# Optimization experiments

Hardware: AMD Instinct MI355X
Metric: run time of the kernel (lower is better)

The kernel has to match this reference:

```python
import jax, jax.numpy as jnp
import numpy as np

EMBED_DIM = 1024
NUM_HEADS = 16
HEAD_DIM = EMBED_DIM // NUM_HEADS

def setup_inputs() -> dict:
    key = jax.random.key(0)
    k1, k2, k3 = jax.random.split(key, 3)
    x = jax.random.normal(k1, (4, 2048, EMBED_DIM), dtype=jnp.float32)
    # Linear weights stored as [out, in] like torch; we apply x @ W.T
    W_qkv = jax.random.normal(k2, (3 * EMBED_DIM, EMBED_DIM), dtype=jnp.float32) * (EMBED_DIM ** -0.5)
    W_proj = jax.random.normal(k3, (EMBED_DIM, EMBED_DIM), dtype=jnp.float32) * (EMBED_DIM ** -0.5)
    return {"x": x, "W_qkv": W_qkv, "W_proj": W_proj}

def reference(x, W_qkv, W_proj):
    B, T, C = x.shape
    H, D = NUM_HEADS, HEAD_DIM
    qkv = x @ W_qkv.T                          # [B,T,3C]
    q, k, v = jnp.split(qkv, 3, axis=-1)
    q = q.reshape(B, T, H, D).transpose(0, 2, 1, 3)  # [B,H,T,D]
    k = k.reshape(B, T, H, D).transpose(0, 2, 1, 3)
    v = v.reshape(B, T, H, D).transpose(0, 2, 1, 3)
    scores = jnp.einsum('bhqd,bhkd->bhqk', q, k) / jnp.sqrt(jnp.asarray(D, x.dtype))
    causal = jnp.tril(jnp.ones((T, T), dtype=bool))
    scores = jnp.where(causal, scores, -jnp.inf)
    weights = jax.nn.softmax(scores, axis=-1)
    out = jnp.einsum('bhqk,bhkd->bhqd', weights, v)  # [B,H,T,D]
    out = out.transpose(0, 2, 1, 3).reshape(B, T, C)
    return out @ W_proj.T
```

## Files before the change

### kernel.cpp

```cpp
#include <hip/hip_runtime.h>

#define T_SEQ 2048
#define NB 4
#define NH 16
#define HD 64
#define CDIM 1024
#define MROWS (NB * T_SEQ)

typedef __attribute__((ext_vector_type(8))) short short8;
typedef __attribute__((ext_vector_type(4))) float floatx4;

static __device__ __forceinline__ unsigned short f2bf(float f) {
  union { float f; unsigned int i; } c; c.f = f;
  return (unsigned short)((c.i + 0x7FFFu + ((c.i >> 16) & 1u)) >> 16);
}
static __device__ __forceinline__ unsigned short f2bf_trunc(float f) {
  union { float f; unsigned int i; } c; c.f = f;
  return (unsigned short)(c.i >> 16);
}

static __device__ __forceinline__ void gl2lds16(const void* g, void* l) {
  __builtin_amdgcn_global_load_lds(
      (const __attribute__((address_space(1))) unsigned int*)g,
      (__attribute__((address_space(3))) unsigned int*)l, 16, 0, 0);
}

#define X4 (MROWS * CDIM / 4)
#define WQ4 (3 * CDIM * CDIM / 4)
#define WP4 (CDIM * CDIM / 4)
__global__ __launch_bounds__(256) void cast3_bf16(const float* __restrict__ x,
                                                  const float* __restrict__ wq,
                                                  const float* __restrict__ wp,
                                                  unsigned short* __restrict__ out) {
  const int i = blockIdx.x * 256 + threadIdx.x;
  const float* src; int off;
  if (i < X4) { src = x; off = i; }
  else if (i < X4 + WQ4) { src = wq; off = i - X4; }
  else { src = wp; off = i - X4 - WQ4; }
  const float4 v = ((const float4*)src)[off];
  ushort4 o;
  o.x = f2bf(v.x); o.y = f2bf(v.y); o.z = f2bf(v.z); o.w = f2bf(v.w);
  ((ushort4*)out)[i] = o;
}

#define Q_PRESCALE 0.18033688f

#define QNT (CDIM / 64)

__global__ __launch_bounds__(512, 2) void gemm_bf16_qkv256(
    const unsigned short* __restrict__ A,
    const unsigned short* __restrict__ B,
    unsigned short* __restrict__ Oq,
    unsigned short* __restrict__ Ok,
    unsigned short* __restrict__ Ovt,
    const int K)
{
  __shared__ __align__(16) unsigned short As[2][2][128 * 64];
  __shared__ __align__(16) unsigned short Bs[2][2][128 * 64];
  const int tid = threadIdx.x;
  const int w = tid >> 6, l = tid & 63;
  const int quad = l >> 4, l15 = l & 15;
  const int wr = w >> 2, wc = w & 3;
  const int lin = blockIdx.y * 12 + blockIdx.x;
  const int swz = (lin & 7) * 48 + (lin >> 3);
  const int m0 = (swz / 12) * 256, n0 = (swz % 12) * 256;

  const int lrow = l >> 3;
  const int lch = ((l & 7) ^ lrow) * 8;
  const unsigned short* Ag = A + (size_t)(m0 + w * 16 + lrow) * K + lch;
  const unsigned short* Bg = B + (size_t)(n0 + w * 16 + lrow) * K + lch;
  const int ld0 = w * 1024, ld1 = w * 1024 + 512;
  const size_t rsk = (size_t)8 * K;

#define STAGE_A(buf, h, kof) do { \
    gl2lds16(Ag + (size_t)(h) * 128 * K + (kof), &As[buf][h][ld0]); \
    gl2lds16(Ag + (size_t)(h) * 128 * K + rsk + (kof), &As[buf][h][ld1]); } while (0)
#define STAGE_B(buf, h, kof) do { \
    gl2lds16(Bg + (size_t)(h) * 128 * K + (kof), &Bs[buf][h][ld0]); \
    gl2lds16(Bg + (size_t)(h) * 128 * K + rsk + (kof), &Bs[buf][h][ld1]); } while (0)

  const int sw7 = l15 & 7;
  const int co0 = (quad ^ sw7) * 8;
  const int co1 = co0 ^ 32;
  const int fb = l15 * 64;
  const unsigned short* Aw0 = &As[0][wr][0];
  const unsigned short* Aw1 = &As[1][wr][0];
  const unsigned short* Bw0 = &Bs[0][wc >> 1][(wc & 1) * 4096];
  const unsigned short* Bw1 = &Bs[1][wc >> 1][(wc & 1) * 4096];

  floatx4 acc[8][4];
#pragma unroll
  for (int mi = 0; mi < 8; ++mi)
#pragma unroll
    for (int ni = 0; ni < 4; ++ni) acc[mi][ni] = (floatx4){0.f, 0.f, 0.f, 0.f};

  STAGE_A(0, 0, 0); STAGE_A(0, 1, 0); STAGE_B(0, 0, 0); STAGE_B(0, 1, 0);
  STAGE_B(1, 0, 64); STAGE_A(1, 0, 64);
  asm volatile("s_waitcnt vmcnt(4)" ::: "memory");
  __builtin_amdgcn_s_barrier();

#pragma unroll 1
  for (int j = 0; j < QNT; ++j) {
    const int cur = j & 1, nxt = cur ^ 1;
    const unsigned short* Ac = cur ? Aw1 : Aw0;
    const unsigned short* Bc = cur ? Bw1 : Bw0;
    const int kA = (j + 1) * 64, kC = (j + 2) * 64;
    short8 aF[2][4], bL[2][2], bH[2][2];

#pragma unroll
    for (int mi = 0; mi < 4; ++mi) {
      aF[0][mi] = *(const short8*)(Ac + mi * 1024 + fb + co0);
      aF[1][mi] = *(const short8*)(Ac + mi * 1024 + fb + co1);
    }
#pragma unroll
    for (int ni = 0; ni < 2; ++ni) {
      bL[0][ni] = *(const short8*)(Bc + ni * 1024 + fb + co0);
      bL[1][ni] = *(const short8*)(Bc + ni * 1024 + fb + co1);
    }
    if (j + 1 < QNT) STAGE_A(nxt, 1, kA);
    __builtin_amdgcn_s_barrier();
    asm volatile("s_waitcnt lgkmcnt(0)" ::: "memory");
    __builtin_amdgcn_s_setprio(1);
#pragma unroll
    for (int ks = 0; ks < 2; ++ks)
#pragma unroll
      for (int mi = 0; mi < 4; ++mi)
#pragma unroll
        for (int ni = 0; ni < 2; ++ni)
          acc[mi][ni] = __builtin_amdgcn_mfma_f32_16x16x32_bf16(
              bL[ks][ni], aF[ks][mi], acc[mi][ni], 0, 0, 0);
    __builtin_amdgcn_s_setprio(0);
    __builtin_amdgcn_s_barrier();

#pragma unroll
    for (int ni = 0; ni < 2; ++ni) {
      bH[0][ni] = *(const short8*)(Bc + (ni + 2) * 1024 + fb + co0);
      bH[1][ni] = *(const short8*)(Bc + (ni + 2) * 1024 + fb + co1);
    }
    if (j + 1 < QNT) STAGE_B(nxt, 1, kA);
    __builtin_amdgcn_s_barrier();
    asm volatile("s_waitcnt lgkmcnt(0)" ::: "memory");
    __builtin_amdgcn_s_setprio(1);
#pragma unroll
    for (int ks = 0; ks < 2; ++ks)
#pragma unroll
      for (int mi = 0; mi < 4; ++mi)
#pragma unroll
        for (int ni = 0; ni < 2; ++ni)
          acc[mi][ni + 2] = __builtin_amdgcn_mfma_f32_16x16x32_bf16(
              bH[ks][ni], aF[ks][mi], acc[mi][ni + 2], 0, 0, 0);
    __builtin_amdgcn_s_setprio(0);
    __builtin_amdgcn_s_barrier();

#pragma unroll
    for (int mi = 0; mi < 4; ++mi) {
      aF[0][mi] = *(const short8*)(Ac + (mi + 4) * 1024 + fb + co0);
      aF[1][mi] = *(const short8*)(Ac + (mi + 4) * 1024 + fb + co1);
    }
    if (j + 2 < QNT) STAGE_B(cur, 0, kC);
    __builtin_amdgcn_s_barrier();
    asm volatile("s_waitcnt lgkmcnt(0)" ::: "memory");
    __builtin_amdgcn_s_setprio(1);
#pragma unroll
    for (int ks = 0; ks < 2; ++ks)
#pragma unroll
      for (int mi = 0; mi < 4; ++mi)
#pragma unroll
        for (int ni = 0; ni < 2; ++ni)
          acc[mi + 4][ni] = __builtin_amdgcn_mfma_f32_16x16x32_bf16(
              bL[ks][ni], aF[ks][mi], acc[mi + 4][ni], 0, 0, 0);
    __builtin_amdgcn_s_setprio(0);
    __builtin_amdgcn_s_barrier();

    if (j + 2 < QNT) {
      STAGE_A(cur, 0, kC);
      asm volatile("s_waitcnt vmcnt(4)" ::: "memory");
    } else {
      asm volatile("s_waitcnt vmcnt(0)" ::: "memory");
    }
    __builtin_amdgcn_s_barrier();
    __builtin_amdgcn_s_setprio(1);
#pragma unroll
    for (int ks = 0; ks < 2; ++ks)
#pragma unroll
      for (int mi = 0; mi < 4; ++mi)
#pragma unroll
        for (int ni = 0; ni < 2; ++ni)
          acc[mi + 4][ni + 2] = __builtin_amdgcn_mfma_f32_16x16x32_bf16(
              bH[ks][ni], aF[ks][mi], acc[mi + 4][ni + 2], 0, 0, 0);
    __builtin_amdgcn_s_setprio(0);
    __builtin_amdgcn_s_barrier();
  }
#undef STAGE_A
#undef STAGE_B

  const int which = n0 >> 10;
  if (which < 2) {
    unsigned short* dst = (which == 0) ? Oq : Ok;
    const float sc = (which == 0) ? Q_PRESCALE : 1.0f;
#pragma unroll
    for (int ni = 0; ni < 4; ++ni) {
      const int n = n0 + wc * 64 + ni * 16 + quad * 4;
      const int h = (n >> 6) & (NH - 1), d = n & (HD - 1);
#pragma unroll
      for (int mi = 0; mi < 8; ++mi) {
        const int m = m0 + wr * 128 + mi * 16 + l15;
        const int b = m >> 11, t = m & (T_SEQ - 1);
        ushort4 pk;
        pk.x = f2bf(acc[mi][ni][0] * sc); pk.y = f2bf(acc[mi][ni][1] * sc);
        pk.z = f2bf(acc[mi][ni][2] * sc); pk.w = f2bf(acc[mi][ni][3] * sc);
        *(ushort4*)(dst + (((size_t)(b * NH + h) * T_SEQ + t) << 6) + d) = pk;
      }
    }
  } else {
#pragma unroll
    for (int ni = 0; ni < 4; ++ni) {
      const int nb = n0 + wc * 64 + ni * 16 + quad * 4;
      const int h = (nb >> 6) & (NH - 1);
#pragma unroll
      for (int mi = 0; mi < 8; ++mi) {
        const int m = m0 + wr * 128 + mi * 16 + l15;
        const int b = m >> 11, t = m & (T_SEQ - 1);
#pragma unroll
        for (int r = 0; r < 4; ++r) {
          const int d = (nb + r) & (HD - 1);
          Ovt[((size_t)((b * NH + h) * HD + d) << 11) + t] = f2bf(acc[mi][ni][r]);
        }
      }
    }
  }
}

__global__ __launch_bounds__(256, 2) void gemm_bf16_proj128(
    const unsigned short* __restrict__ A,
    const unsigned short* __restrict__ B,
    float* __restrict__ O,
    const int K)
{
  __shared__ __align__(16) unsigned short As[2][128 * 64];
  __shared__ __align__(16) unsigned short Bs[3][128 * 64];
  const int tid = threadIdx.x;
  const int w = tid >> 6, l = tid & 63;
  const int quad = l >> 4, l15 = l & 15;
  const int wr = w >> 1, wc = w & 1;
  const int lin = blockIdx.y * 8 + blockIdx.x;
  const int swz = (lin & 7) * 64 + (lin >> 3);
  const int m0 = (swz >> 3) * 128, n0 = (swz & 7) * 128;

  const int st_row = tid >> 3;
  const int st_sch = ((tid & 7) ^ (st_row & 7)) * 8;
  const unsigned short* Ast = A + (size_t)(m0 + st_row) * K + st_sch;
  const unsigned short* Bst = B + (size_t)(n0 + st_row) * K + st_sch;
  const int dst8 = tid * 8;

#define PSTG_A(buf, kof) do { \
    gl2lds16(Ast + (kof), &As[buf][dst8]); \
    gl2lds16(Ast + (size_t)32 * K + (kof), &As[buf][2048 + dst8]); \
    gl2lds16(Ast + (size_t)64 * K + (kof), &As[buf][4096 + dst8]); \
    gl2lds16(Ast + (size_t)96 * K + (kof), &As[buf][6144 + dst8]); } while (0)
#define PSTG_B(buf, kof) do { \
    gl2lds16(Bst + (kof), &Bs[buf][dst8]); \
    gl2lds16(Bst + (size_t)32 * K + (kof), &Bs[buf][2048 + dst8]); \
    gl2lds16(Bst + (size_t)64 * K + (kof), &Bs[buf][4096 + dst8]); \
    gl2lds16(Bst + (size_t)96 * K + (kof), &Bs[buf][6144 + dst8]); } while (0)

  const int sw7 = l15 & 7;
  const int co0 = (quad ^ sw7) * 8;
  const int co1 = co0 ^ 32;
  const unsigned short* Aw0 = &As[0][wr * 4096 + l15 * 64];
  const unsigned short* Aw1 = &As[1][wr * 4096 + l15 * 64];
  const unsigned short* Bw0 = &Bs[0][wc * 4096 + l15 * 64];
  const unsigned short* Bw1 = &Bs[1][wc * 4096 + l15 * 64];
  const unsigned short* Bw2 = &Bs[2][wc * 4096 + l15 * 64];

  floatx4 acc[4][4];
#pragma unroll
  for (int mi = 0; mi < 4; ++mi)
#pragma unroll
    for (int ni = 0; ni < 4; ++ni) acc[mi][ni] = (floatx4){0.f, 0.f, 0.f, 0.f};

  PSTG_A(0, 0); PSTG_B(0, 0); PSTG_B(1, 64);
  asm volatile("s_waitcnt vmcnt(4)" ::: "memory");
  __builtin_amdgcn_s_barrier();

  int jm3 = 0;
#pragma unroll 1
  for (int j = 0; j < QNT; ++j) {
    const int cur = j & 1, nxt = cur ^ 1;
    const unsigned short* Ac = cur ? Aw1 : Aw0;
    const unsigned short* Bc = (jm3 == 0) ? Bw0 : (jm3 == 1) ? Bw1 : Bw2;
    const int tb = (jm3 >= 1) ? jm3 - 1 : 2;
    short8 aF[2][4], bL[2][2], bH[2][2];

#pragma unroll
    for (int mi = 0; mi < 4; ++mi) {
      aF[0][mi] = *(const short8*)(Ac + mi * 1024 + co0);
      aF[1][mi] = *(const short8*)(Ac + mi * 1024 + co1);
    }
#pragma unroll
    for (int ni = 0; ni < 2; ++ni) {
      bL[0][ni] = *(const short8*)(Bc + ni * 1024 + co0);
      bL[1][ni] = *(const short8*)(Bc + ni * 1024 + co1);
      bH[0][ni] = *(const short8*)(Bc + (ni + 2) * 1024 + co0);
      bH[1][ni] = *(const short8*)(Bc + (ni + 2) * 1024 + co1);
    }
    if (j + 1 < QNT) PSTG_A(nxt, (j + 1) * 64);
    asm volatile("s_waitcnt lgkmcnt(0)" ::: "memory");
    __builtin_amdgcn_s_setprio(1);
#pragma unroll
    for (int ks = 0; ks < 2; ++ks)
#pragma unroll
      for (int mi = 0; mi < 4; ++mi)
#pragma unroll
        for (int ni = 0; ni < 2; ++ni)
          acc[mi][ni] = __builtin_amdgcn_mfma_f32_16x16x32_bf16(
              bL[ks][ni], aF[ks][mi], acc[mi][ni], 0, 0, 0);
    __builtin_amdgcn_s_setprio(0);

    if (j + 2 < QNT) PSTG_B(tb, (j + 2) * 64);
    __builtin_amdgcn_s_setprio(1);
#pragma unroll
    for (int ks = 0; ks < 2; ++ks)
#pragma unroll
      for (int mi = 0; mi < 4; ++mi)
#pragma unroll
        for (int ni = 0; ni < 2; ++ni)
          acc[mi][ni + 2] = __builtin_amdgcn_mfma_f32_16x16x32_bf16(
              bH[ks][ni], aF[ks][mi], acc[mi][ni + 2], 0, 0, 0);
    __builtin_amdgcn_s_setprio(0);
    if (j + 2 < QNT) asm volatile("s_waitcnt vmcnt(4)" ::: "memory");
    else             asm volatile("s_waitcnt vmcnt(0)" ::: "memory");
    __builtin_amdgcn_s_barrier();
    jm3 = (jm3 == 2) ? 0 : jm3 + 1;
  }
#undef PSTG_A
#undef PSTG_B

#pragma unroll
  for (int ni = 0; ni < 4; ++ni) {
    const int n = n0 + wc * 64 + ni * 16 + quad * 4;
#pragma unroll
    for (int mi = 0; mi < 4; ++mi) {
      const int m = m0 + wr * 64 + mi * 16 + l15;
      *(float4*)(O + (size_t)m * CDIM + n) =
          make_float4(acc[mi][ni][0], acc[mi][ni][1], acc[mi][ni][2], acc[mi][ni][3]);
    }
  }
}

#define TK 64
#define PTP 72

__global__ __launch_bounds__(512) void attn_mfma(
    const unsigned short* __restrict__ Q,
    const unsigned short* __restrict__ K,
    const unsigned short* __restrict__ Vt,
    unsigned short* __restrict__ O)
{
  __shared__ unsigned short Ks[2][TK * HD];
  __shared__ unsigned short Vts[2][HD * TK];
  __shared__ unsigned short Pt[8][16 * PTP];
  const int tid = threadIdx.x;
  const int w = tid >> 6, l = tid & 63;
  const int quad = l >> 4, l15 = l & 15;
  const int drow = 8 * w + (l >> 3);
  const int dch = ((l & 7) ^ (l >> 3)) * 8;
  const int sw7 = l15 & 7;

  const int bh = blockIdx.x & 63;
  const int pp = blockIdx.x >> 6;
  const int b = bh >> 4, h = bh & 15;
  const size_t hoff = (size_t)bh * T_SEQ * HD;
  const unsigned short* Qh = Q + hoff;
  const unsigned short* Kdma = K + hoff + (size_t)drow * HD + dch;
  const unsigned short* Vdma = Vt + hoff + ((size_t)drow << 11) + dch;
  const int wb = w * 512;

  short8 ones;
#pragma unroll
  for (int j = 0; j < 8; ++j) ones[j] = (short)0x3F80;

#pragma unroll 1
  for (int ii = 0; ii < 2; ++ii) {
    const int qtile = ii ? pp : (15 - pp);
    const int qw = qtile * 128 + w * 16;

    short8 qf[2];
    {
      const int qrow = qw + l15;
      qf[0] = *(const short8*)(Qh + (size_t)qrow * HD + quad * 8);
      qf[1] = *(const short8*)(Qh + (size_t)qrow * HD + 32 + quad * 8);
    }

    floatx4 Of[4];
#pragma unroll
    for (int dc = 0; dc < 4; ++dc) Of[dc] = (floatx4){0.f, 0.f, 0.f, 0.f};
    floatx4 lacc = (floatx4){0.f, 0.f, 0.f, 0.f};

    const int nkt = 2 * qtile + 2;
    __syncthreads();
    gl2lds16(Kdma, &Ks[0][wb]);
    gl2lds16(Vdma, &Vts[0][wb]);

    for (int kt = 0; kt < nkt; ++kt) {
      const int kt0 = kt * TK;
      const int cur = kt & 1, nxt = 1 - cur;
      __syncthreads();
      if (kt + 1 < nkt) {
        gl2lds16(Kdma + (size_t)(kt0 + TK) * HD, &Ks[nxt][wb]);
        gl2lds16(Vdma + kt0 + TK, &Vts[nxt][wb]);
      }

      if (qw + 15 >= kt0) {
        floatx4 Sf[4];
#pragma unroll
        for (int cb = 0; cb < 4; ++cb) {
          Sf[cb] = (floatx4){0.f, 0.f, 0.f, 0.f};
          const int krow = cb * 16 + l15;
#pragma unroll
          for (int h2 = 0; h2 < 2; ++h2) {
            const int ch = (h2 * 4 + quad) ^ sw7;
            const short8 kf = *(const short8*)&Ks[cur][krow * 64 + ch * 8];
            Sf[cb] = __builtin_amdgcn_mfma_f32_16x16x32_bf16(kf, qf[h2], Sf[cb], 0, 0, 0);
          }
        }
        const bool full = (kt0 + 63 <= qw);
        const int q = qw + l15;
#pragma unroll
        for (int cb = 0; cb < 4; ++cb) {
          const int key0 = kt0 + cb * 16 + quad * 4;
          ushort4 pk;
          if (full) {
            pk.x = f2bf_trunc(exp2f(Sf[cb][0]));
            pk.y = f2bf_trunc(exp2f(Sf[cb][1]));
            pk.z = f2bf_trunc(exp2f(Sf[cb][2]));
            pk.w = f2bf_trunc(exp2f(Sf[cb][3]));
          } else {
            pk.x = (key0 + 0 > q) ? 0 : f2bf_trunc(exp2f(Sf[cb][0]));
            pk.y = (key0 + 1 > q) ? 0 : f2bf_trunc(exp2f(Sf[cb][1]));
            pk.z = (key0 + 2 > q) ? 0 : f2bf_trunc(exp2f(Sf[cb][2]));
            pk.w = (key0 + 3 > q) ? 0 : f2bf_trunc(exp2f(Sf[cb][3]));
          }
          *(ushort4*)&Pt[w][l15 * PTP + cb * 16 + quad * 4] = pk;
        }
#pragma unroll
        for (int kg = 0; kg < 2; ++kg) {
          const short8 ptf = *(const short8*)&Pt[w][l15 * PTP + kg * 32 + quad * 8];
          lacc = __builtin_amdgcn_mfma_f32_16x16x32_bf16(ones, ptf, lacc, 0, 0, 0);
#pragma unroll
          for (int dc = 0; dc < 4; ++dc) {
            const int vrow = dc * 16 + l15;
            const int ch = (kg * 4 + quad) ^ sw7;
            const short8 vf = *(const short8*)&Vts[cur][vrow * 64 + ch * 8];
            Of[dc] = __builtin_amdgcn_mfma_f32_16x16x32_bf16(vf, ptf, Of[dc], 0, 0, 0);
          }
        }
      }
    }

    const float inv = 1.f / lacc[0];
    const int q = qw + l15;
    unsigned short* orow = O + (size_t)(b * T_SEQ + q) * CDIM + h * HD + quad * 4;
#pragma unroll
    for (int dc = 0; dc < 4; ++dc) {
      ushort4 ov;
      ov.x = f2bf(Of[dc][0] * inv); ov.y = f2bf(Of[dc][1] * inv);
      ov.z = f2bf(Of[dc][2] * inv); ov.w = f2bf(Of[dc][3] * inv);
      *(ushort4*)(orow + dc * 16) = ov;
    }
  }
}

extern "C" void kernel_launch(void* const* d_in, const int* in_sizes, int n_in,
                              void* d_out, int out_size, void* d_ws, size_t ws_size,
                              hipStream_t stream) {
  const float* x     = (const float*)d_in[0];
  const float* Wqkv  = (const float*)d_in[1];
  const float* Wproj = (const float*)d_in[2];
  float* out = (float*)d_out;

  const size_t XSZ = (size_t)MROWS * CDIM;
  const size_t WQSZ = (size_t)3 * CDIM * CDIM;
  const size_t WPSZ = (size_t)CDIM * CDIM;
  unsigned short* xb  = (unsigned short*)d_ws;
  unsigned short* wqb = xb + XSZ;
  unsigned short* wpb = wqb + WQSZ;
  unsigned short* qbuf = wpb + WPSZ;
  unsigned short* kbuf = qbuf + XSZ;
  unsigned short* vtbuf = kbuf + XSZ;
  unsigned short* abuf = vtbuf + XSZ;

  cast3_bf16<<<(X4 + WQ4 + WP4) / 256, 256, 0, stream>>>(x, Wqkv, Wproj, xb);

  dim3 g1(3 * CDIM / 256, MROWS / 256);
  gemm_bf16_qkv256<<<g1, 512, 0, stream>>>(xb, wqb, qbuf, kbuf, vtbuf, CDIM);

  attn_mfma<<<512, 512, 0, stream>>>(qbuf, kbuf, vtbuf, abuf);

  dim3 g3(CDIM / 128, MROWS / 128);
  gemm_bf16_proj128<<<g3, 256, 0, stream>>>(abuf, wpb, out, CDIM);
}
```

Measured before the change: 246.8 us.

## Load projection GEMM B operand directly from global into registers

The output projection GEMM no longer stages the weight tile through LDS. Each wave now loads its B fragments straight from global memory into registers, double-buffered across k-tiles. The A tile is still staged in LDS. This cuts LDS use and LDS read traffic, which may allow higher occupancy. The cost is uncoalesced 16-byte global loads with their latency exposed in registers, plus higher register pressure from the two B fragment buffers.

```diff
diff --git a/kernel.cpp b/kernel.cpp
--- a/kernel.cpp
+++ b/kernel.cpp
@@ -231,14 +231,13 @@
   }
 }
 
-__global__ __launch_bounds__(256, 2) void gemm_bf16_proj128(
+__global__ __launch_bounds__(256, 2) void gemm_bf16_projBG(
     const unsigned short* __restrict__ A,
     const unsigned short* __restrict__ B,
     float* __restrict__ O,
     const int K)
 {
   __shared__ __align__(16) unsigned short As[2][128 * 64];
-  __shared__ __align__(16) unsigned short Bs[3][128 * 64];
   const int tid = threadIdx.x;
   const int w = tid >> 6, l = tid & 63;
   const int quad = l >> 4, l15 = l & 15;
@@ -250,7 +249,6 @@
   const int st_row = tid >> 3;
   const int st_sch = ((tid & 7) ^ (st_row & 7)) * 8;
   const unsigned short* Ast = A + (size_t)(m0 + st_row) * K + st_sch;
-  const unsigned short* Bst = B + (size_t)(n0 + st_row) * K + st_sch;
   const int dst8 = tid * 8;
 
 #define PSTG_A(buf, kof) do { \
@@ -258,20 +256,21 @@
     gl2lds16(Ast + (size_t)32 * K + (kof), &As[buf][2048 + dst8]); \
     gl2lds16(Ast + (size_t)64 * K + (kof), &As[buf][4096 + dst8]); \
     gl2lds16(Ast + (size_t)96 * K + (kof), &As[buf][6144 + dst8]); } while (0)
-#define PSTG_B(buf, kof) do { \
-    gl2lds16(Bst + (kof), &Bs[buf][dst8]); \
-    gl2lds16(Bst + (size_t)32 * K + (kof), &Bs[buf][2048 + dst8]); \
-    gl2lds16(Bst + (size_t)64 * K + (kof), &Bs[buf][4096 + dst8]); \
-    gl2lds16(Bst + (size_t)96 * K + (kof), &Bs[buf][6144 + dst8]); } while (0)
 
   const int sw7 = l15 & 7;
   const int co0 = (quad ^ sw7) * 8;
   const int co1 = co0 ^ 32;
   const unsigned short* Aw0 = &As[0][wr * 4096 + l15 * 64];
   const unsigned short* Aw1 = &As[1][wr * 4096 + l15 * 64];
-  const unsigned short* Bw0 = &Bs[0][wc * 4096 + l15 * 64];
-  const unsigned short* Bw1 = &Bs[1][wc * 4096 + l15 * 64];
-  const unsigned short* Bw2 = &Bs[2][wc * 4096 + l15 * 64];
+
+  const unsigned short* Bg2 = B + (size_t)(n0 + wc * 64 + l15) * K + quad * 8;
+
+#define LOADB(dst, J) do { \
+    _Pragma("unroll") \
+    for (int ni = 0; ni < 4; ++ni) { \
+      dst[0][ni] = *(const short8*)(Bg2 + (size_t)(ni * 16) * K + (J) * 64); \
+      dst[1][ni] = *(const short8*)(Bg2 + (size_t)(ni * 16) * K + (J) * 64 + 32); \
+    } } while (0)
 
   floatx4 acc[4][4];
 #pragma unroll
@@ -279,62 +278,45 @@
 #pragma unroll
     for (int ni = 0; ni < 4; ++ni) acc[mi][ni] = (floatx4){0.f, 0.f, 0.f, 0.f};
 
-  PSTG_A(0, 0); PSTG_B(0, 0); PSTG_B(1, 64);
-  asm volatile("s_waitcnt vmcnt(4)" ::: "memory");
+  short8 bA[2][4], bB[2][4];
+
+  PSTG_A(0, 0);
+  LOADB(bA, 0);
+  asm volatile("s_waitcnt vmcnt(0)" ::: "memory");
   __builtin_amdgcn_s_barrier();
 
-  int jm3 = 0;
+#define KTILE(ACUR, ANXT, BCUR, BNXT, J) do { \
+    short8 aF[2][4]; \
+    _Pragma("unroll") \
+    for (int mi = 0; mi < 4; ++mi) { \
+      aF[0][mi] = *(const short8*)((ACUR) + mi * 1024 + co0); \
+      aF[1][mi] = *(const short8*)((ACUR) + mi * 1024 + co1); \
+    } \
+    if ((J) + 1 < QNT) { PSTG_A(ANXT, ((J) + 1) * 64); LOADB(BNXT, (J) + 1); } \
+    asm volatile("s_waitcnt lgkmcnt(0)" ::: "memory"); \
+    __builtin_amdgcn_s_setprio(1); \
+    _Pragma("unroll") \
+    for (int ks = 0; ks < 2; ++ks) \
+      _Pragma("unroll") \
+      for (int mi = 0; mi < 4; ++mi) \
+        _Pragma("unroll") \
+        for (int ni = 0; ni < 4; ++ni) \
+          acc[mi][ni] = __builtin_amdgcn_mfma_f32_16x16x32_bf16( \
+              BCUR[ks][ni], aF[ks][mi], acc[mi][ni], 0, 0, 0); \
+    __builtin_amdgcn_s_setprio(0); \
+    if ((J) + 1 < QNT) asm volatile("s_waitcnt vmcnt(8)" ::: "memory"); \
+    else               asm volatile("s_waitcnt vmcnt(0)" ::: "memory"); \
+    __builtin_amdgcn_s_barrier(); \
+  } while (0)
+
 #pragma unroll 1
-  for (int j = 0; j < QNT; ++j) {
-    const int cur = j & 1, nxt = cur ^ 1;
-    const unsigned short* Ac = cur ? Aw1 : Aw0;
-    const unsigned short* Bc = (jm3 == 0) ? Bw0 : (jm3 == 1) ? Bw1 : Bw2;
-    const int tb = (jm3 >= 1) ? jm3 - 1 : 2;
-    short8 aF[2][4], bL[2][2], bH[2][2];
-
-#pragma unroll
-    for (int mi = 0; mi < 4; ++mi) {
-      aF[0][mi] = *(const short8*)(Ac + mi * 1024 + co0);
-      aF[1][mi] = *(const short8*)(Ac + mi * 1024 + co1);
-    }
-#pragma unroll
-    for (int ni = 0; ni < 2; ++ni) {
-      bL[0][ni] = *(const short8*)(Bc + ni * 1024 + co0);
-      bL[1][ni] = *(const short8*)(Bc + ni * 1024 + co1);
-      bH[0][ni] = *(const short8*)(Bc + (ni + 2) * 1024 + co0);
-      bH[1][ni] = *(const short8*)(Bc + (ni + 2) * 1024 + co1);
-    }
-    if (j + 1 < QNT) PSTG_A(nxt, (j + 1) * 64);
-    asm volatile("s_waitcnt lgkmcnt(0)" ::: "memory");
-    __builtin_amdgcn_s_setprio(1);
-#pragma unroll
-    for (int ks = 0; ks < 2; ++ks)
-#pragma unroll
-      for (int mi = 0; mi < 4; ++mi)
-#pragma unroll
-        for (int ni = 0; ni < 2; ++ni)
-          acc[mi][ni] = __builtin_amdgcn_mfma_f32_16x16x32_bf16(
-              bL[ks][ni], aF[ks][mi], acc[mi][ni], 0, 0, 0);
-    __builtin_amdgcn_s_setprio(0);
-
-    if (j + 2 < QNT) PSTG_B(tb, (j + 2) * 64);
-    __builtin_amdgcn_s_setprio(1);
-#pragma unroll
-    for (int ks = 0; ks < 2; ++ks)
-#pragma unroll
-      for (int mi = 0; mi < 4; ++mi)
-#pragma unroll
-        for (int ni = 0; ni < 2; ++ni)
-          acc[mi][ni + 2] = __builtin_amdgcn_mfma_f32_16x16x32_bf16(
-              bH[ks][ni], aF[ks][mi], acc[mi][ni + 2], 0, 0, 0);
-    __builtin_amdgcn_s_setprio(0);
-    if (j + 2 < QNT) asm volatile("s_waitcnt vmcnt(4)" ::: "memory");
-    else             asm volatile("s_waitcnt vmcnt(0)" ::: "memory");
-    __builtin_amdgcn_s_barrier();
-    jm3 = (jm3 == 2) ? 0 : jm3 + 1;
+  for (int jj = 0; jj < QNT; jj += 2) {
+    KTILE(Aw0, 1, bA, bB, jj);
+    KTILE(Aw1, 0, bB, bA, jj + 1);
   }
+#undef KTILE
+#undef LOADB
 #undef PSTG_A
-#undef PSTG_B
 
 #pragma unroll
   for (int ni = 0; ni < 4; ++ni) {
@@ -498,5 +480,5 @@
   attn_mfma<<<512, 512, 0, stream>>>(qbuf, kbuf, vtbuf, abuf);
 
   dim3 g3(CDIM / 128, MROWS / 128);
-  gemm_bf16_proj128<<<g3, 256, 0, stream>>>(abuf, wpb, out, CDIM);
-}
+  gemm_bf16_projBG<<<g3, 256, 0, stream>>>(abuf, wpb, out, CDIM);
+}
```

New measurement: 266.8 us. +8.1%, slower.
